# Kernel tuning notes

Measured on AMD Instinct MI355X. Metric: run time of the kernel, lower is better.

Reference implementation:

```python
import jax, jax.numpy as jnp
import numpy as np

N = 16_777_216  # total elements
B = 16_384      # number of segments (graphs/batches)
EPS = 1e-12


def setup_inputs() -> dict:
    key = jax.random.key(0)
    k1, k2, k3 = jax.random.split(key, 3)
    preds = jax.random.normal(k1, (N,), dtype=jnp.float32)
    target = jax.random.normal(k2, (N,), dtype=jnp.float32)
    batch_map = jnp.sort(jax.random.randint(k3, (N,), 0, B, dtype=jnp.int64))
    return {"preds": preds, "target": target, "batch_map": batch_map}


def reference(preds, target, batch_map):
    # per-segment squared norms and dot product (three scatter-sums in torch)
    seg = lambda v: jax.ops.segment_sum(v, batch_map, num_segments=B,
                                        indices_are_sorted=True)
    preds_norm = jnp.sqrt(seg(preds * preds))      # [B]
    target_norm = jnp.sqrt(seg(target * target))   # [B]
    dot_product = seg(preds * target)              # [B]
    cosine = dot_product / jnp.maximum(preds_norm * target_norm, EPS)
    return jnp.mean(1.0 - cosine)
```

## Files before the change

kernel.cpp:

```cpp
#include <hip/hip_runtime.h>

#define NSEG 16384
#define EPS  1e-12f

__global__ void bsearch_kernel(const int* __restrict__ map,
                               int* __restrict__ start, int n) {
    int b = blockIdx.x * blockDim.x + threadIdx.x;
    if (b > NSEG) return;
    int est = b << 10;
    int wlo = est - 20000; if (wlo < 0) wlo = 0;
    int whi = est + 20000; if (whi > n) whi = n;
    int lo = wlo, hi = whi;
    while (lo < hi) { int mid = (lo + hi) >> 1; if (map[mid] < b) lo = mid + 1; else hi = mid; }
    bool bad = (lo == wlo && wlo > 0 && map[wlo - 1] >= b) ||
               (lo == whi && whi < n && map[whi] < b);
    if (bad) {
        lo = 0; hi = n;
        while (lo < hi) { int mid = (lo + hi) >> 1; if (map[mid] < b) lo = mid + 1; else hi = mid; }
    }
    start[b] = lo;
}

__device__ __forceinline__ float dpp_add(float x, int ctrl);
#define DPP_ADD_IMPL(CTRL)                                                     \
    __device__ __forceinline__ float dpp_add_##CTRL(float x) {                 \
        int y = __builtin_amdgcn_update_dpp(0, __float_as_int(x), CTRL,        \
                                            0xf, 0xf, true);                   \
        return x + __int_as_float(y);                                          \
    }
DPP_ADD_IMPL(0x111)
DPP_ADD_IMPL(0x112)
DPP_ADD_IMPL(0x114)
DPP_ADD_IMPL(0x118)
DPP_ADD_IMPL(0x142)
DPP_ADD_IMPL(0x143)

#define DPPRED3(x, y, z)                                         \
    do {                                                         \
        x = dpp_add_0x111(x); y = dpp_add_0x111(y); z = dpp_add_0x111(z); \
        x = dpp_add_0x112(x); y = dpp_add_0x112(y); z = dpp_add_0x112(z); \
        x = dpp_add_0x114(x); y = dpp_add_0x114(y); z = dpp_add_0x114(z); \
        x = dpp_add_0x118(x); y = dpp_add_0x118(y); z = dpp_add_0x118(z); \
        x = dpp_add_0x142(x); y = dpp_add_0x142(y); z = dpp_add_0x142(z); \
        x = dpp_add_0x143(x); y = dpp_add_0x143(y); z = dpp_add_0x143(z); \
    } while (0)

#define LOADC(P, T, CIDX)                                                      \
    do {                                                                       \
        const int vb_ = (CIDX) << 8;                                           \
        _Pragma("unroll")                                                      \
        for (int k_ = 0; k_ < 4; ++k_) P[k_] = p4[vb_ + k_ * 64 + lane];       \
        _Pragma("unroll")                                                      \
        for (int k_ = 0; k_ < 4; ++k_) T[k_] = t4[vb_ + k_ * 64 + lane];       \
    } while (0)

#define COLX(pe, te, eidx)                                                     \
    { const float px_ = (pe), tx_ = (te);                                      \
      const float cxx_ = px_ * px_, cyy_ = tx_ * tx_, cxy_ = px_ * tx_;        \
      const bool i0_ = (eidx) < b1_;                                           \
      const bool i2_ = (eidx) >= b2_;                                          \
      q0 += i0_ ? cxx_ : 0.f; r0 += i0_ ? cyy_ : 0.f; u0 += i0_ ? cxy_ : 0.f;  \
      q2 += i2_ ? cxx_ : 0.f; r2 += i2_ ? cyy_ : 0.f; u2 += i2_ ? cxy_ : 0.f;  \
      const bool i1_ = !i0_ && !i2_;                                           \
      q1 += i1_ ? cxx_ : 0.f; r1 += i1_ ? cyy_ : 0.f; u1 += i1_ ? cxy_ : 0.f; }

#define DO_CHUNK(P, T, CIDX)                                                   \
    do {                                                                       \
        const int hb_ = (CIDX) << 10;                                          \
        const unsigned long long mm_ = __ballot(sv <= hb_);                    \
        const int kk_ = 63 - __builtin_clzll(mm_);                             \
        const int mh_ = base_id + kk_;                                         \
        const int sA_ = __builtin_amdgcn_readlane(sv, kk_);                    \
        const int k1_ = kk_ + 1 > 63 ? 63 : kk_ + 1;                           \
        const int k2_ = kk_ + 2 > 63 ? 63 : kk_ + 2;                           \
        const int b1_ = __builtin_amdgcn_readlane(sv, k1_);                    \
        const int b2_ = __builtin_amdgcn_readlane(sv, k2_);                    \
        float q0=0,r0=0,u0=0, q1=0,r1=0,u1=0, q2=0,r2=0,u2=0;                  \
        _Pragma("unroll")                                                      \
        for (int g_ = 0; g_ < 4; ++g_) {                                       \
            const float4 pv = P[g_], tv = T[g_];                               \
            const int G_ = hb_ + g_ * 256, Ge_ = G_ + 256;                     \
            if (Ge_ <= b1_) {                                                  \
                q0 += pv.x*pv.x + pv.y*pv.y + pv.z*pv.z + pv.w*pv.w;           \
                r0 += tv.x*tv.x + tv.y*tv.y + tv.z*tv.z + tv.w*tv.w;           \
                u0 += pv.x*tv.x + pv.y*tv.y + pv.z*tv.z + pv.w*tv.w;           \
            } else if (G_ >= b1_ && Ge_ <= b2_) {                              \
                q1 += pv.x*pv.x + pv.y*pv.y + pv.z*pv.z + pv.w*pv.w;           \
                r1 += tv.x*tv.x + tv.y*tv.y + tv.z*tv.z + tv.w*tv.w;           \
                u1 += pv.x*tv.x + pv.y*tv.y + pv.z*tv.z + pv.w*tv.w;           \
            } else if (G_ >= b2_) {                                            \
                q2 += pv.x*pv.x + pv.y*pv.y + pv.z*pv.z + pv.w*pv.w;           \
                r2 += tv.x*tv.x + tv.y*tv.y + tv.z*tv.z + tv.w*tv.w;           \
                u2 += pv.x*tv.x + pv.y*tv.y + pv.z*tv.z + pv.w*tv.w;           \
            } else {                                                           \
                const int e0_ = hb_ + (g_ * 64 + lane) * 4;                    \
                COLX(pv.x, tv.x, e0_ + 0)                                      \
                COLX(pv.y, tv.y, e0_ + 1)                                      \
                COLX(pv.z, tv.z, e0_ + 2)                                      \
                COLX(pv.w, tv.w, e0_ + 3)                                      \
            }                                                                  \
        }                                                                      \
        const int nloc_ = (b1_ < hb_ + 1024) + (b2_ < hb_ + 1024);             \
        DPPRED3(q0, r0, u0);                                                   \
        if (nloc_ >= 1) DPPRED3(q1, r1, u1);                                   \
        if (nloc_ >= 2) DPPRED3(q2, r2, u2);                                   \
        if (lane == 63) {                                                      \
            wb[mh_ * 3 + ((CIDX) - (sA_ >> 10))] = make_float4(q0, r0, u0, 0.f); \
            if (nloc_ >= 1) wb[(mh_ + 1) * 3] = make_float4(q1, r1, u1, 0.f);  \
            if (nloc_ >= 2) wb[(mh_ + 2) * 3] = make_float4(q2, r2, u2, 0.f);  \
        }                                                                      \
    } while (0)

__global__ __launch_bounds__(256) void seg_main(const float4* __restrict__ p4,
                                                const float4* __restrict__ t4,
                                                const int* __restrict__ start,
                                                float4* __restrict__ wb) {
    const int lane = threadIdx.x & 63;
    const int wv   = (blockIdx.x << 2) + (threadIdx.x >> 6);
    const int c0   = wv << 2;

    const int base_id = c0 - 20;
    int gidx = base_id + lane;
    gidx = gidx < 0 ? 0 : (gidx > NSEG ? NSEG : gidx);
    const int sv = start[gidx];

    float4 PA[4], TA[4], PB[4], TB[4];
    LOADC(PA, TA, c0);
    LOADC(PB, TB, c0 + 1);

    DO_CHUNK(PA, TA, c0);
    LOADC(PA, TA, c0 + 2);
    DO_CHUNK(PB, TB, c0 + 1);
    LOADC(PB, TB, c0 + 3);
    DO_CHUNK(PA, TA, c0 + 2);
    DO_CHUNK(PB, TB, c0 + 3);
}

__global__ void finalize1(const float4* __restrict__ wb,
                          const int* __restrict__ start,
                          float* __restrict__ part) {
    float local = 0.0f;
    for (int s = blockIdx.x * blockDim.x + threadIdx.x; s < NSEG;
         s += gridDim.x * blockDim.x) {
        const int s0 = start[s], s1 = start[s + 1];
        float cosv = 0.0f;
        if (s1 > s0) {
            float4 v = wb[s * 3];
            const int r0 = s0 >> 10, r1 = (s1 - 1) >> 10;
            if (r1 > r0)     { float4 u = wb[s * 3 + 1]; v.x += u.x; v.y += u.y; v.z += u.z; }
            if (r1 > r0 + 1) { float4 u = wb[s * 3 + 2]; v.x += u.x; v.y += u.y; v.z += u.z; }
            cosv = v.z / fmaxf(sqrtf(v.x) * sqrtf(v.y), EPS);
        }
        local += 1.0f - cosv;
    }
    #pragma unroll
    for (int off = 32; off > 0; off >>= 1) local += __shfl_down(local, off);
    __shared__ float wsum[4];
    const int wd = threadIdx.x >> 6;
    if ((threadIdx.x & 63) == 0) wsum[wd] = local;
    __syncthreads();
    if (threadIdx.x == 0)
        part[blockIdx.x] = wsum[0] + wsum[1] + wsum[2] + wsum[3];
}

__global__ void finalize2(const float* __restrict__ part,
                          float* __restrict__ out, int npart) {
    float local = (threadIdx.x < npart) ? part[threadIdx.x] : 0.0f;
    #pragma unroll
    for (int off = 32; off > 0; off >>= 1) local += __shfl_down(local, off);
    if (threadIdx.x == 0) out[0] = local / (float)NSEG;
}

extern "C" void kernel_launch(void* const* d_in, const int* in_sizes, int n_in,
                              void* d_out, int out_size, void* d_ws, size_t ws_size,
                              hipStream_t stream) {
    const float4* p = (const float4*)d_in[0];
    const float4* t = (const float4*)d_in[1];
    const int*    s = (const int*)d_in[2];
    const int n = in_sizes[0];

    int*    start = (int*)d_ws;
    float4* wb    = (float4*)((char*)d_ws + 65552);
    float*  part  = (float*)((char*)d_ws + 65552 + 786432);

    bsearch_kernel<<<65, 256, 0, stream>>>(s, start, n);
    seg_main<<<1024, 256, 0, stream>>>(p, t, start, wb);
    finalize1<<<64, 256, 0, stream>>>(wb, start, part);
    finalize2<<<1, 64, 0, stream>>>(part, (float*)d_out, 64);
}
```

Measured before the change: 37.28 us.

## Fuse segment-start search into main kernel and finalize into one last-block kernel

Drops the separate binary-search kernel: each block of the main kernel computes the segment starts it needs into shared memory, and this overlaps with its first global loads. The main kernel also writes a per-segment partial-count into the spare float4 lane, so finalization no longer reads the start array. The two finalize kernels merge into one, using an atomic ticket so the last block does the final sum. Launches drop from four to two, at the cost of redundant binary searches per block and atomics and fences in the finalize step.

New measurement: 54.75 us. 1.47x slower.

```diff
diff --git a/kernel.cpp b/kernel.cpp
--- a/kernel.cpp
+++ b/kernel.cpp
@@ -3,10 +3,7 @@
 #define NSEG 16384
 #define EPS  1e-12f
 
-__global__ void bsearch_kernel(const int* __restrict__ map,
-                               int* __restrict__ start, int n) {
-    int b = blockIdx.x * blockDim.x + threadIdx.x;
-    if (b > NSEG) return;
+__device__ __forceinline__ int wlb(const int* __restrict__ map, int n, int b) {
     int est = b << 10;
     int wlo = est - 20000; if (wlo < 0) wlo = 0;
     int whi = est + 20000; if (whi > n) whi = n;
@@ -18,10 +15,9 @@
         lo = 0; hi = n;
         while (lo < hi) { int mid = (lo + hi) >> 1; if (map[mid] < b) lo = mid + 1; else hi = mid; }
     }
-    start[b] = lo;
+    return lo;
 }
 
-__device__ __forceinline__ float dpp_add(float x, int ctrl);
 #define DPP_ADD_IMPL(CTRL)                                                     \
     __device__ __forceinline__ float dpp_add_##CTRL(float x) {                 \
         int y = __builtin_amdgcn_update_dpp(0, __float_as_int(x), CTRL,        \
@@ -35,14 +31,14 @@
 DPP_ADD_IMPL(0x142)
 DPP_ADD_IMPL(0x143)
 
-#define DPPRED3(x, y, z)                                         \
-    do {                                                         \
-        x = dpp_add_0x111(x); y = dpp_add_0x111(y); z = dpp_add_0x111(z); \
-        x = dpp_add_0x112(x); y = dpp_add_0x112(y); z = dpp_add_0x112(z); \
-        x = dpp_add_0x114(x); y = dpp_add_0x114(y); z = dpp_add_0x114(z); \
-        x = dpp_add_0x118(x); y = dpp_add_0x118(y); z = dpp_add_0x118(z); \
-        x = dpp_add_0x142(x); y = dpp_add_0x142(y); z = dpp_add_0x142(z); \
-        x = dpp_add_0x143(x); y = dpp_add_0x143(y); z = dpp_add_0x143(z); \
+#define DPPRED3(x, y, z)                                                       \
+    do {                                                                       \
+        x = dpp_add_0x111(x); y = dpp_add_0x111(y); z = dpp_add_0x111(z);      \
+        x = dpp_add_0x112(x); y = dpp_add_0x112(y); z = dpp_add_0x112(z);      \
+        x = dpp_add_0x114(x); y = dpp_add_0x114(y); z = dpp_add_0x114(z);      \
+        x = dpp_add_0x118(x); y = dpp_add_0x118(y); z = dpp_add_0x118(z);      \
+        x = dpp_add_0x142(x); y = dpp_add_0x142(y); z = dpp_add_0x142(z);      \
+        x = dpp_add_0x143(x); y = dpp_add_0x143(y); z = dpp_add_0x143(z);      \
     } while (0)
 
 #define LOADC(P, T, CIDX)                                                      \
@@ -73,8 +69,10 @@
         const int sA_ = __builtin_amdgcn_readlane(sv, kk_);                    \
         const int k1_ = kk_ + 1 > 63 ? 63 : kk_ + 1;                           \
         const int k2_ = kk_ + 2 > 63 ? 63 : kk_ + 2;                           \
+        const int k3_ = kk_ + 3 > 63 ? 63 : kk_ + 3;                           \
         const int b1_ = __builtin_amdgcn_readlane(sv, k1_);                    \
         const int b2_ = __builtin_amdgcn_readlane(sv, k2_);                    \
+        const int b3_ = __builtin_amdgcn_readlane(sv, k3_);                    \
         float q0=0,r0=0,u0=0, q1=0,r1=0,u1=0, q2=0,r2=0,u2=0;                  \
         _Pragma("unroll")                                                      \
         for (int g_ = 0; g_ < 4; ++g_) {                                       \
@@ -105,28 +103,41 @@
         if (nloc_ >= 1) DPPRED3(q1, r1, u1);                                   \
         if (nloc_ >= 2) DPPRED3(q2, r2, u2);                                   \
         if (lane == 63) {                                                      \
-            wb[mh_ * 3 + ((CIDX) - (sA_ >> 10))] = make_float4(q0, r0, u0, 0.f); \
-            if (nloc_ >= 1) wb[(mh_ + 1) * 3] = make_float4(q1, r1, u1, 0.f);  \
-            if (nloc_ >= 2) wb[(mh_ + 2) * 3] = make_float4(q2, r2, u2, 0.f);  \
+            const int slot0_ = (CIDX) - (sA_ >> 10);                           \
+            const float w0_ = (slot0_ == 0)                                    \
+                ? (float)(((b1_ - 1) >> 10) - (CIDX) + 1) : 0.0f;              \
+            wb[mh_ * 3 + slot0_] = make_float4(q0, r0, u0, w0_);               \
+            if (nloc_ >= 1) wb[(mh_ + 1) * 3] = make_float4(q1, r1, u1,        \
+                (float)(((b2_ - 1) >> 10) - (CIDX) + 1));                      \
+            if (nloc_ >= 2) wb[(mh_ + 2) * 3] = make_float4(q2, r2, u2,        \
+                (float)(((b3_ - 1) >> 10) - (CIDX) + 1));                      \
         }                                                                      \
     } while (0)
 
 __global__ __launch_bounds__(256) void seg_main(const float4* __restrict__ p4,
                                                 const float4* __restrict__ t4,
-                                                const int* __restrict__ start,
-                                                float4* __restrict__ wb) {
+                                                const int* __restrict__ map,
+                                                float4* __restrict__ wb,
+                                                int* __restrict__ ticket, int n) {
     const int lane = threadIdx.x & 63;
-    const int wv   = (blockIdx.x << 2) + (threadIdx.x >> 6);
+    const int wid  = threadIdx.x >> 6;
+    const int wv   = (blockIdx.x << 2) + wid;
     const int c0   = wv << 2;
-
     const int base_id = c0 - 20;
-    int gidx = base_id + lane;
-    gidx = gidx < 0 ? 0 : (gidx > NSEG ? NSEG : gidx);
-    const int sv = start[gidx];
 
     float4 PA[4], TA[4], PB[4], TB[4];
     LOADC(PA, TA, c0);
     LOADC(PB, TB, c0 + 1);
+
+    __shared__ int lds_start[128];
+    if (threadIdx.x < 128) {
+        int id = (blockIdx.x << 4) - 32 + threadIdx.x;
+        id = id < 0 ? 0 : (id > NSEG ? NSEG : id);
+        lds_start[threadIdx.x] = wlb(map, n, id);
+    }
+    if (blockIdx.x == 0 && threadIdx.x == 0) *ticket = 0;
+    __syncthreads();
+    const int sv = lds_start[(wid << 2) + 12 + lane];
 
     DO_CHUNK(PA, TA, c0);
     LOADC(PA, TA, c0 + 2);
@@ -136,39 +147,36 @@
     DO_CHUNK(PB, TB, c0 + 3);
 }
 
-__global__ void finalize1(const float4* __restrict__ wb,
-                          const int* __restrict__ start,
-                          float* __restrict__ part) {
-    float local = 0.0f;
-    for (int s = blockIdx.x * blockDim.x + threadIdx.x; s < NSEG;
-         s += gridDim.x * blockDim.x) {
-        const int s0 = start[s], s1 = start[s + 1];
-        float cosv = 0.0f;
-        if (s1 > s0) {
-            float4 v = wb[s * 3];
-            const int r0 = s0 >> 10, r1 = (s1 - 1) >> 10;
-            if (r1 > r0)     { float4 u = wb[s * 3 + 1]; v.x += u.x; v.y += u.y; v.z += u.z; }
-            if (r1 > r0 + 1) { float4 u = wb[s * 3 + 2]; v.x += u.x; v.y += u.y; v.z += u.z; }
-            cosv = v.z / fmaxf(sqrtf(v.x) * sqrtf(v.y), EPS);
-        }
-        local += 1.0f - cosv;
-    }
+__global__ __launch_bounds__(256) void fin_fused(const float4* __restrict__ wb,
+                                                 float* __restrict__ part,
+                                                 int* __restrict__ ticket,
+                                                 float* __restrict__ out) {
+    const int s = blockIdx.x * 256 + threadIdx.x;
+    float4 v = wb[s * 3];
+    const int ns = (int)v.w;
+    if (ns >= 2) { float4 u = wb[s * 3 + 1]; v.x += u.x; v.y += u.y; v.z += u.z; }
+    if (ns >= 3) { float4 u = wb[s * 3 + 2]; v.x += u.x; v.y += u.y; v.z += u.z; }
+    float local = 1.0f - v.z / fmaxf(sqrtf(v.x) * sqrtf(v.y), EPS);
+
     #pragma unroll
     for (int off = 32; off > 0; off >>= 1) local += __shfl_down(local, off);
-    __shared__ float wsum[4];
-    const int wd = threadIdx.x >> 6;
-    if ((threadIdx.x & 63) == 0) wsum[wd] = local;
+    __shared__ float ws4[4];
+    __shared__ int is_last;
+    if ((threadIdx.x & 63) == 0) ws4[threadIdx.x >> 6] = local;
     __syncthreads();
-    if (threadIdx.x == 0)
-        part[blockIdx.x] = wsum[0] + wsum[1] + wsum[2] + wsum[3];
-}
-
-__global__ void finalize2(const float* __restrict__ part,
-                          float* __restrict__ out, int npart) {
-    float local = (threadIdx.x < npart) ? part[threadIdx.x] : 0.0f;
-    #pragma unroll
-    for (int off = 32; off > 0; off >>= 1) local += __shfl_down(local, off);
-    if (threadIdx.x == 0) out[0] = local / (float)NSEG;
+    if (threadIdx.x == 0) {
+        part[blockIdx.x] = ws4[0] + ws4[1] + ws4[2] + ws4[3];
+        __threadfence();
+        is_last = (atomicAdd(ticket, 1) == 63);
+    }
+    __syncthreads();
+    if (is_last && threadIdx.x < 64) {
+        __threadfence();
+        float pv = atomicAdd(&part[threadIdx.x], 0.0f);
+        #pragma unroll
+        for (int off = 32; off > 0; off >>= 1) pv += __shfl_down(pv, off);
+        if (threadIdx.x == 0) out[0] = pv / (float)NSEG;
+    }
 }
 
 extern "C" void kernel_launch(void* const* d_in, const int* in_sizes, int n_in,
@@ -179,12 +187,10 @@
     const int*    s = (const int*)d_in[2];
     const int n = in_sizes[0];
 
-    int*    start = (int*)d_ws;
-    float4* wb    = (float4*)((char*)d_ws + 65552);
-    float*  part  = (float*)((char*)d_ws + 65552 + 786432);
+    float4* wb     = (float4*)d_ws;
+    float*  part   = (float*)((char*)d_ws + 786432);
+    int*    ticket = (int*)((char*)d_ws + 786432 + 256);
 
-    bsearch_kernel<<<65, 256, 0, stream>>>(s, start, n);
-    seg_main<<<1024, 256, 0, stream>>>(p, t, start, wb);
-    finalize1<<<64, 256, 0, stream>>>(wb, start, part);
-    finalize2<<<1, 64, 0, stream>>>(part, (float*)d_out, 64);
+    seg_main<<<1024, 256, 0, stream>>>(p, t, s, wb, ticket, n);
+    fin_fused<<<64, 256, 0, stream>>>(wb, part, ticket, (float*)d_out);
 }
```
